# Optimization experiments

Measured on AMD Instinct MI355X. Metric: run time of the kernel, lower is better.

Reference implementation:

```python
import jax, jax.numpy as jnp
import numpy as np

H = 1024   # hidden size
E = 8      # num experts
B, S = 4, 2048


def setup_inputs() -> dict:
    key = jax.random.key(0)
    k1, k2, k3, k4 = jax.random.split(key, 4)
    x = jax.random.normal(k1, (B, S, H), dtype=jnp.float32)
    wg = jax.random.normal(k2, (H, E), dtype=jnp.float32) * 0.02      # gate weight
    W = jax.random.normal(k3, (E, H, H), dtype=jnp.float32) * 0.02    # expert Linear weights (out, in) per expert
    b = jax.random.normal(k4, (E, H), dtype=jnp.float32) * 0.02       # expert Linear biases
    return {"x": x, "wg": wg, "W": W, "b": b}


def reference(x, wg, W, b):
    Bb, Ss, Hh = x.shape
    Ee = wg.shape[1]
    T = Bb * Ss
    C = T // Ee  # capacity (capacity_factor = 1.0, top-1)

    xt = x.reshape(T, Hh)
    logits = xt @ wg                                   # [T, E]
    probs = jax.nn.softmax(logits, axis=-1)            # [T, E]
    idx = jnp.argmax(probs, axis=-1)                   # [T] top-1 expert
    mask = jax.nn.one_hot(idx, Ee, dtype=xt.dtype)     # [T, E]

    # position of each token within its expert's queue (0-based)
    locations = jnp.cumsum(mask, axis=0) - mask        # [T, E]
    # drop tokens over capacity
    mask = mask * (locations < C).astype(xt.dtype)
    gate = jnp.sum(probs * mask, axis=-1)              # [T] gate prob (0 if dropped)
    loc_s = jnp.sum(locations * mask, axis=-1).astype(jnp.int32)  # [T]
    loc_oh = jax.nn.one_hot(loc_s, C, dtype=xt.dtype)  # [T, C]

    dispatch = mask[:, :, None] * loc_oh[:, None, :]   # [T, E, C]
    combine = gate[:, None, None] * dispatch           # [T, E, C]

    # dispatch tokens -> per-expert buffers [E, C, H]
    exp_in = jnp.einsum('tec,th->ech', dispatch, xt)
    # per-expert Linear: y = x @ W_e^T + b_e
    exp_out = jnp.einsum('ech,efh->ecf', exp_in, W) + b[:, None, :]
    # combine back to tokens, scaled by gate prob
    out = jnp.einsum('tec,ecf->tf', combine, exp_out)  # [T, H]
    return out.reshape(Bb, Ss, Hh)
```

## Files before the change

kernel.cpp:

```cpp
#include <hip/hip_runtime.h>

#define H 1024
#define E 8
#define T 8192
#define CAP 1024

typedef __bf16 bf16x8 __attribute__((ext_vector_type(8)));
typedef float  f32x4  __attribute__((ext_vector_type(4)));
typedef unsigned short u16;

__device__ __forceinline__ u16 f2bf(float f) {
    union { float f; unsigned u; } v; v.f = f;
    unsigned r = v.u + 0x7FFFu + ((v.u >> 16) & 1u);
    return (u16)(r >> 16);
}

typedef __attribute__((address_space(1))) const void* gas_t;
typedef __attribute__((address_space(3))) void* las_t;
__device__ __forceinline__ void gld16(const void* g, void* l) {
    __builtin_amdgcn_global_load_lds((gas_t)g, (las_t)l, 16, 0, 0);
}

#define GATE_BLOCKS 512
#define CVT_BLOCKS  1536
#define WGP 1028

__global__ __launch_bounds__(256) void gatecvt_kernel(
    const float* __restrict__ x, const float* __restrict__ wg,
    const float* __restrict__ W,
    int* __restrict__ eid, float* __restrict__ gate,
    u16* __restrict__ xbf, u16* __restrict__ Wbf) {
    __shared__ float wgs[E * WGP];
    const int tid = threadIdx.x;

    if (blockIdx.x >= GATE_BLOCKS) {
        int i = (blockIdx.x - GATE_BLOCKS) * 256 + tid;
        const int n4 = E * H * H / 4;
        const int stride = CVT_BLOCKS * 256;
        for (; i < n4; i += stride) {
            float4 v = ((const float4*)W)[i];
            ushort4 o;
            o.x = f2bf(v.x); o.y = f2bf(v.y); o.z = f2bf(v.z); o.w = f2bf(v.w);
            ((ushort4*)Wbf)[i] = o;
        }
        return;
    }

    for (int i = tid; i < E * H; i += 256)
        wgs[(i & 7) * WGP + (i >> 3)] = wg[i];
    __syncthreads();

    const int wv = tid >> 6, lane = tid & 63;
    const int tbase = blockIdx.x * 16 + wv * 4;
    const int h00 = lane * 4;

    float a[4][8];
    #pragma unroll
    for (int j = 0; j < 4; ++j)
        #pragma unroll
        for (int e = 0; e < 8; ++e) a[j][e] = 0.f;

    #pragma unroll
    for (int q = 0; q < 4; ++q) {
        const int h0 = q * 256 + h00;
        float4 xv[4];
        #pragma unroll
        for (int j = 0; j < 4; ++j)
            xv[j] = *(const float4*)(x + (size_t)(tbase + j) * H + h0);
        #pragma unroll
        for (int j = 0; j < 4; ++j) {
            ushort4 o;
            o.x = f2bf(xv[j].x); o.y = f2bf(xv[j].y);
            o.z = f2bf(xv[j].z); o.w = f2bf(xv[j].w);
            *(ushort4*)(xbf + (size_t)(tbase + j) * H + h0) = o;
        }
        #pragma unroll
        for (int e = 0; e < 8; ++e) {
            const float4 w4 = *(const float4*)&wgs[e * WGP + h0];
            #pragma unroll
            for (int j = 0; j < 4; ++j)
                a[j][e] += xv[j].x * w4.x + xv[j].y * w4.y
                         + xv[j].z * w4.z + xv[j].w * w4.w;
        }
    }

    const bool b0 = lane & 1, b1 = lane & 2, b2 = lane & 4;
    const int elane = ((lane & 1) << 2) | (lane & 2) | ((lane >> 2) & 1);

    #pragma unroll
    for (int j = 0; j < 4; ++j) {
        float* A = a[j];
        #pragma unroll
        for (int k = 0; k < 4; ++k) {
            float t = b0 ? A[k] : A[k + 4];
            t = __shfl_xor(t, 1);
            A[k] = (b0 ? A[k + 4] : A[k]) + t;
        }
        #pragma unroll
        for (int k = 0; k < 2; ++k) {
            float t = b1 ? A[k] : A[k + 2];
            t = __shfl_xor(t, 2);
            A[k] = (b1 ? A[k + 2] : A[k]) + t;
        }
        {
            float t = b2 ? A[0] : A[1];
            t = __shfl_xor(t, 4);
            A[0] = (b2 ? A[1] : A[0]) + t;
        }
        float v = A[0];
        v += __shfl_xor(v, 8); v += __shfl_xor(v, 16); v += __shfl_xor(v, 32);
        float m = v; int mi = elane;
        #pragma unroll
        for (int off = 1; off <= 4; off <<= 1) {
            float om = __shfl_xor(m, off);
            int   oi = __shfl_xor(mi, off);
            if (om > m || (om == m && oi < mi)) { m = om; mi = oi; }
        }
        float s = expf(v - m);
        s += __shfl_xor(s, 1); s += __shfl_xor(s, 2); s += __shfl_xor(s, 4);
        if (lane == 0) {
            eid[tbase + j]  = mi;
            gate[tbase + j] = 1.0f / s;
        }
    }
}

#define TPT 32
__global__ __launch_bounds__(256) void scan_kernel(
    const int* __restrict__ eid, float* __restrict__ gate,
    int* __restrict__ perm) {
    __shared__ int cnt[256][E];
    __shared__ int base[256][E];
    __shared__ int part[E][8];
    const int tid = threadIdx.x;

    for (int i = tid; i < E * CAP; i += 256) perm[i] = -1;

    const int t0 = tid * TPT;
    int c[E];
    #pragma unroll
    for (int e = 0; e < E; ++e) c[e] = 0;
    for (int i = 0; i < TPT; ++i) {
        const int ei = eid[t0 + i];
        #pragma unroll
        for (int e = 0; e < E; ++e) c[e] += (ei == e);
    }
    #pragma unroll
    for (int e = 0; e < E; ++e) cnt[tid][e] = c[e];
    __syncthreads();
    if (tid < 64) {
        const int e = tid >> 3, j = tid & 7;
        int s = 0;
        for (int i = j * 32; i < j * 32 + 32; ++i) s += cnt[i][e];
        part[e][j] = s;
    }
    __syncthreads();
    if (tid < E) {
        int run = 0;
        #pragma unroll
        for (int j = 0; j < 8; ++j) { int v = part[tid][j]; part[tid][j] = run; run += v; }
    }
    __syncthreads();
    if (tid < 64) {
        const int e = tid >> 3, j = tid & 7;
        int run = part[e][j];
        for (int i = j * 32; i < j * 32 + 32; ++i) { base[i][e] = run; run += cnt[i][e]; }
    }
    __syncthreads();
    #pragma unroll
    for (int e = 0; e < E; ++e) c[e] = base[tid][e];
    for (int i = 0; i < TPT; ++i) {
        const int t = t0 + i;
        const int ei = eid[t];
        int pos = 0;
        #pragma unroll
        for (int e = 0; e < E; ++e) if (ei == e) pos = c[e]++;
        if (pos < CAP) perm[ei * CAP + pos] = t;
        else gate[t] = 0.f;
    }
}

#define BK 64
__global__ __launch_bounds__(256) void moe_gemm_bf(
    const u16* __restrict__ xbf, const u16* __restrict__ Wbf,
    const float* __restrict__ bias, const int* __restrict__ perm,
    const float* __restrict__ gate, float* __restrict__ out) {
    __shared__ __align__(16) u16 As[128 * BK];
    __shared__ __align__(16) u16 Bs[128 * BK];
    __shared__ int   perm_s[128];
    __shared__ float gate_s[128];

    const int e   = blockIdx.z;
    const int mb  = blockIdx.y;
    const int fb  = blockIdx.x;
    const int tid = threadIdx.x;

    if (tid < 128) {
        const int t = perm[e * CAP + mb * 128 + tid];
        perm_s[tid] = t;
        gate_s[tid] = (t >= 0) ? gate[t] : 0.f;
    }
    __syncthreads();

    const int lane = tid & 63;
    const int wv = tid >> 6;
    const int wm = wv >> 1, wn = wv & 1;
    const int l16 = lane & 15, quad = lane >> 4;

    const int rl  = lane >> 3;
    const int cch = lane & 7;
    const int gch = cch ^ rl;
    const u16* ga[4]; const u16* gb[4];
    u16* la[4]; u16* lb[4];
    #pragma unroll
    for (int q = 0; q < 4; ++q) {
        const int r = (wv * 4 + q) * 8 + rl;
        const int tA = perm_s[r];
        const int tok = tA >= 0 ? tA : 0;
        ga[q] = xbf + (size_t)tok * H + gch * 8;
        gb[q] = Wbf + (size_t)e * H * H + (size_t)(fb * 128 + r) * H + gch * 8;
        la[q] = &As[(wv * 4 + q) * 512 + lane * 8];
        lb[q] = &Bs[(wv * 4 + q) * 512 + lane * 8];
    }

    f32x4 acc[4][4] = {};

    for (int kt = 0; kt < H / BK; ++kt) {
        __syncthreads();
        #pragma unroll
        for (int q = 0; q < 4; ++q) {
            gld16(ga[q], la[q]);
            gld16(gb[q], lb[q]);
            ga[q] += BK; gb[q] += BK;
        }
        __syncthreads();
        #pragma unroll
        for (int s = 0; s < 2; ++s) {
            bf16x8 af[4], bfr[4];
            const int cc = (s * 4 + quad) ^ (l16 & 7);
            #pragma unroll
            for (int i = 0; i < 4; ++i) {
                af[i]  = *(const bf16x8*)&As[(wm * 64 + i * 16 + l16) * BK + cc * 8];
                bfr[i] = *(const bf16x8*)&Bs[(wn * 64 + i * 16 + l16) * BK + cc * 8];
            }
            #pragma unroll
            for (int mi = 0; mi < 4; ++mi)
                #pragma unroll
                for (int ni = 0; ni < 4; ++ni)
                    acc[mi][ni] = __builtin_amdgcn_mfma_f32_16x16x32_bf16(
                        af[mi], bfr[ni], acc[mi][ni], 0, 0, 0);
        }
    }

    float bv[4];
    #pragma unroll
    for (int ni = 0; ni < 4; ++ni)
        bv[ni] = bias[e * H + fb * 128 + wn * 64 + ni * 16 + l16];

    #pragma unroll
    for (int mi = 0; mi < 4; ++mi) {
        #pragma unroll
        for (int r = 0; r < 4; ++r) {
            const int rowl = wm * 64 + mi * 16 + quad * 4 + r;
            const int t = perm_s[rowl];
            if (t < 0) continue;
            const float g = gate_s[rowl];
            float* orow = out + (size_t)t * H + fb * 128 + wn * 64;
            #pragma unroll
            for (int ni = 0; ni < 4; ++ni)
                orow[ni * 16 + l16] = g * (acc[mi][ni][r] + bv[ni]);
        }
    }
}

__global__ __launch_bounds__(256) void zero_dropped(
    const float* __restrict__ gate, float* __restrict__ out) {
    const int wave = (blockIdx.x * blockDim.x + threadIdx.x) >> 6;
    const int lane = threadIdx.x & 63;
    if (gate[wave] != 0.f) return;
    float4 z = make_float4(0.f, 0.f, 0.f, 0.f);
    float4* o = (float4*)(out + (size_t)wave * H);
    #pragma unroll
    for (int i = 0; i < H / 4 / 64; ++i) o[i * 64 + lane] = z;
}

extern "C" void kernel_launch(void* const* d_in, const int* in_sizes, int n_in,
                              void* d_out, int out_size, void* d_ws, size_t ws_size,
                              hipStream_t stream) {
    const float* x    = (const float*)d_in[0];
    const float* wg   = (const float*)d_in[1];
    const float* W    = (const float*)d_in[2];
    const float* bias = (const float*)d_in[3];
    float* out = (float*)d_out;

    int*   eid  = (int*)d_ws;
    float* gate = (float*)((char*)d_ws + (size_t)T * 4);
    int*   perm = (int*)((char*)d_ws + (size_t)T * 8);
    u16*   xbf  = (u16*)((char*)d_ws + (size_t)T * 12);
    u16*   Wbf  = xbf + (size_t)T * H;

    gatecvt_kernel<<<GATE_BLOCKS + CVT_BLOCKS, 256, 0, stream>>>(
        x, wg, W, eid, gate, xbf, Wbf);
    scan_kernel<<<1, 256, 0, stream>>>(eid, gate, perm);
    moe_gemm_bf<<<dim3(8, 8, 8), 256, 0, stream>>>(xbf, Wbf, bias, perm, gate, out);
    zero_dropped<<<T / 4, 256, 0, stream>>>(gate, out);
}
```

Before: 156.5 us.

## Pre-transpose gate weights, double K tile, fold dropped-row zeroing into GEMM grid

Adds a tiny kernel that transposes the gate weight so gatecvt reads it straight from global memory instead of staging 32KB into LDS per block. The GEMM now loads a 128-wide K slice per barrier pair, halving the sync count at the cost of twice the LDS. The separate zero_dropped launch is removed and its work becomes an extra z-slice of the GEMM grid. The LDS growth may cut occupancy, and the new wgt_kernel adds a launch of its own.

Result: no change. 159.3 us (+1.8%).

```diff
diff --git a/kernel.cpp b/kernel.cpp
--- a/kernel.cpp
+++ b/kernel.cpp
@@ -21,16 +21,25 @@
     __builtin_amdgcn_global_load_lds((gas_t)g, (las_t)l, 16, 0, 0);
 }
 
+__global__ __launch_bounds__(256) void wgt_kernel(
+    const float* __restrict__ wg, float* __restrict__ wgT) {
+    const int h = blockIdx.x * 256 + threadIdx.x;
+    float4 lo = *(const float4*)(wg + h * E);
+    float4 hi = *(const float4*)(wg + h * E + 4);
+    wgT[0 * H + h] = lo.x; wgT[1 * H + h] = lo.y;
+    wgT[2 * H + h] = lo.z; wgT[3 * H + h] = lo.w;
+    wgT[4 * H + h] = hi.x; wgT[5 * H + h] = hi.y;
+    wgT[6 * H + h] = hi.z; wgT[7 * H + h] = hi.w;
+}
+
 #define GATE_BLOCKS 512
 #define CVT_BLOCKS  1536
-#define WGP 1028
 
 __global__ __launch_bounds__(256) void gatecvt_kernel(
-    const float* __restrict__ x, const float* __restrict__ wg,
+    const float* __restrict__ x, const float* __restrict__ wgT,
     const float* __restrict__ W,
     int* __restrict__ eid, float* __restrict__ gate,
     u16* __restrict__ xbf, u16* __restrict__ Wbf) {
-    __shared__ float wgs[E * WGP];
     const int tid = threadIdx.x;
 
     if (blockIdx.x >= GATE_BLOCKS) {
@@ -46,10 +55,6 @@
         return;
     }
 
-    for (int i = tid; i < E * H; i += 256)
-        wgs[(i & 7) * WGP + (i >> 3)] = wg[i];
-    __syncthreads();
-
     const int wv = tid >> 6, lane = tid & 63;
     const int tbase = blockIdx.x * 16 + wv * 4;
     const int h00 = lane * 4;
@@ -76,7 +81,7 @@
         }
         #pragma unroll
         for (int e = 0; e < 8; ++e) {
-            const float4 w4 = *(const float4*)&wgs[e * WGP + h0];
+            const float4 w4 = *(const float4*)(wgT + e * H + h0);
             #pragma unroll
             for (int j = 0; j < 4; ++j)
                 a[j][e] += xv[j].x * w4.x + xv[j].y * w4.y
@@ -180,20 +185,32 @@
     }
 }
 
-#define BK 64
 __global__ __launch_bounds__(256) void moe_gemm_bf(
     const u16* __restrict__ xbf, const u16* __restrict__ Wbf,
     const float* __restrict__ bias, const int* __restrict__ perm,
     const float* __restrict__ gate, float* __restrict__ out) {
-    __shared__ __align__(16) u16 As[128 * BK];
-    __shared__ __align__(16) u16 Bs[128 * BK];
+    __shared__ __align__(16) u16 As[2][128 * 64];
+    __shared__ __align__(16) u16 Bs[2][128 * 64];
     __shared__ int   perm_s[128];
     __shared__ float gate_s[128];
 
-    const int e   = blockIdx.z;
-    const int mb  = blockIdx.y;
-    const int fb  = blockIdx.x;
     const int tid = threadIdx.x;
+
+    if (blockIdx.z == 8) {
+        const int t = (blockIdx.y * 8 + blockIdx.x) * 128 + (tid >> 1);
+        if (gate[t] == 0.f) {
+            const int half = tid & 1;
+            float4 z = make_float4(0.f, 0.f, 0.f, 0.f);
+            float4* o = (float4*)(out + (size_t)t * H + half * 512);
+            #pragma unroll
+            for (int i = 0; i < 128; ++i) o[i] = z;
+        }
+        return;
+    }
+
+    const int e  = blockIdx.z;
+    const int mb = blockIdx.y;
+    const int fb = blockIdx.x;
 
     if (tid < 128) {
         const int t = perm[e * CAP + mb * 128 + tid];
@@ -211,7 +228,6 @@
     const int cch = lane & 7;
     const int gch = cch ^ rl;
     const u16* ga[4]; const u16* gb[4];
-    u16* la[4]; u16* lb[4];
     #pragma unroll
     for (int q = 0; q < 4; ++q) {
         const int r = (wv * 4 + q) * 8 + rl;
@@ -219,37 +235,40 @@
         const int tok = tA >= 0 ? tA : 0;
         ga[q] = xbf + (size_t)tok * H + gch * 8;
         gb[q] = Wbf + (size_t)e * H * H + (size_t)(fb * 128 + r) * H + gch * 8;
-        la[q] = &As[(wv * 4 + q) * 512 + lane * 8];
-        lb[q] = &Bs[(wv * 4 + q) * 512 + lane * 8];
     }
 
     f32x4 acc[4][4] = {};
 
-    for (int kt = 0; kt < H / BK; ++kt) {
+    for (int kt = 0; kt < H / 128; ++kt) {
         __syncthreads();
         #pragma unroll
-        for (int q = 0; q < 4; ++q) {
-            gld16(ga[q], la[q]);
-            gld16(gb[q], lb[q]);
-            ga[q] += BK; gb[q] += BK;
-        }
+        for (int hb = 0; hb < 2; ++hb)
+            #pragma unroll
+            for (int q = 0; q < 4; ++q) {
+                gld16(ga[q] + hb * 64, &As[hb][(wv * 4 + q) * 512 + lane * 8]);
+                gld16(gb[q] + hb * 64, &Bs[hb][(wv * 4 + q) * 512 + lane * 8]);
+            }
+        #pragma unroll
+        for (int q = 0; q < 4; ++q) { ga[q] += 128; gb[q] += 128; }
         __syncthreads();
         #pragma unroll
-        for (int s = 0; s < 2; ++s) {
-            bf16x8 af[4], bfr[4];
-            const int cc = (s * 4 + quad) ^ (l16 & 7);
-            #pragma unroll
-            for (int i = 0; i < 4; ++i) {
-                af[i]  = *(const bf16x8*)&As[(wm * 64 + i * 16 + l16) * BK + cc * 8];
-                bfr[i] = *(const bf16x8*)&Bs[(wn * 64 + i * 16 + l16) * BK + cc * 8];
+        for (int hb = 0; hb < 2; ++hb)
+            #pragma unroll
+            for (int s = 0; s < 2; ++s) {
+                bf16x8 af[4], bfr[4];
+                const int cc = (s * 4 + quad) ^ (l16 & 7);
+                #pragma unroll
+                for (int i = 0; i < 4; ++i) {
+                    af[i]  = *(const bf16x8*)&As[hb][(wm * 64 + i * 16 + l16) * 64 + cc * 8];
+                    bfr[i] = *(const bf16x8*)&Bs[hb][(wn * 64 + i * 16 + l16) * 64 + cc * 8];
+                }
+                #pragma unroll
+                for (int mi = 0; mi < 4; ++mi)
+                    #pragma unroll
+                    for (int ni = 0; ni < 4; ++ni)
+                        acc[mi][ni] = __builtin_amdgcn_mfma_f32_16x16x32_bf16(
+                            af[mi], bfr[ni], acc[mi][ni], 0, 0, 0);
             }
-            #pragma unroll
-            for (int mi = 0; mi < 4; ++mi)
-                #pragma unroll
-                for (int ni = 0; ni < 4; ++ni)
-                    acc[mi][ni] = __builtin_amdgcn_mfma_f32_16x16x32_bf16(
-                        af[mi], bfr[ni], acc[mi][ni], 0, 0, 0);
-        }
     }
 
     float bv[4];
@@ -271,17 +290,6 @@
                 orow[ni * 16 + l16] = g * (acc[mi][ni][r] + bv[ni]);
         }
     }
-}
-
-__global__ __launch_bounds__(256) void zero_dropped(
-    const float* __restrict__ gate, float* __restrict__ out) {
-    const int wave = (blockIdx.x * blockDim.x + threadIdx.x) >> 6;
-    const int lane = threadIdx.x & 63;
-    if (gate[wave] != 0.f) return;
-    float4 z = make_float4(0.f, 0.f, 0.f, 0.f);
-    float4* o = (float4*)(out + (size_t)wave * H);
-    #pragma unroll
-    for (int i = 0; i < H / 4 / 64; ++i) o[i * 64 + lane] = z;
 }
 
 extern "C" void kernel_launch(void* const* d_in, const int* in_sizes, int n_in,
@@ -296,12 +304,13 @@
     int*   eid  = (int*)d_ws;
     float* gate = (float*)((char*)d_ws + (size_t)T * 4);
     int*   perm = (int*)((char*)d_ws + (size_t)T * 8);
-    u16*   xbf  = (u16*)((char*)d_ws + (size_t)T * 12);
+    float* wgT  = (float*)((char*)d_ws + (size_t)T * 12);
+    u16*   xbf  = (u16*)((char*)d_ws + (size_t)T * 12 + (size_t)E * H * 4);
     u16*   Wbf  = xbf + (size_t)T * H;
 
+    wgt_kernel<<<H / 256, 256, 0, stream>>>(wg, wgT);
     gatecvt_kernel<<<GATE_BLOCKS + CVT_BLOCKS, 256, 0, stream>>>(
-        x, wg, W, eid, gate, xbf, Wbf);
+        x, wgT, W, eid, gate, xbf, Wbf);
     scan_kernel<<<1, 256, 0, stream>>>(eid, gate, perm);
-    moe_gemm_bf<<<dim3(8, 8, 8), 256, 0, stream>>>(xbf, Wbf, bias, perm, gate, out);
-    zero_dropped<<<T / 4, 256, 0, stream>>>(gate, out);
-}
+    moe_gemm_bf<<<dim3(8, 8, 9), 256, 0, stream>>>(xbf, Wbf, bias, perm, gate, out);
+}
```
